# Performance work log

Measured on AMD Instinct MI355X. Metric: run time of the kernel, lower is better.

## Reference

```python
import jax, jax.numpy as jnp
import numpy as np

B, T = 256, 512
LATENT, COND, HID, OUT = 128, 32, 512, 64
IN_DIM = OUT + COND  # LSTM input dim = output_dim + condition_dim


def setup_inputs() -> dict:
    key = jax.random.key(0)
    ks = jax.random.split(key, 14)
    def lin(k, fan_in, shape):
        return jax.random.uniform(k, shape, jnp.float32, -1.0, 1.0) / np.sqrt(fan_in)
    return {
        "latent_vector": jax.random.normal(ks[0], (B, LATENT), jnp.float32),
        "conditions": jax.random.normal(ks[1], (B, COND), jnp.float32),
        "target_sequences": jax.random.normal(ks[2], (B, T, OUT), jnp.float32),
        # latent_to_hidden / latent_to_cell
        "W_lh": lin(ks[3], LATENT, (HID, LATENT)), "b_lh": lin(ks[4], LATENT, (HID,)),
        "W_lc": lin(ks[5], LATENT, (HID, LATENT)), "b_lc": lin(ks[6], LATENT, (HID,)),
        # LSTM weights, torch gate order [i, f, g, o]
        "W_ih": lin(ks[7], HID, (4 * HID, IN_DIM)), "W_hh": lin(ks[8], HID, (4 * HID, HID)),
        "b_ih": lin(ks[9], HID, (4 * HID,)), "b_hh": lin(ks[10], HID, (4 * HID,)),
        # hidden_to_output
        "W_out": lin(ks[11], HID, (OUT, HID)), "b_out": lin(ks[12], HID, (OUT,)),
        "output_lengths": jnp.full((B,), T, dtype=jnp.int32),
    }


def _decode(latent_vector, conditions, target_sequences,
            W_lh, b_lh, W_lc, b_lc, W_ih, W_hh, b_ih, b_hh, W_out, b_out):
    Bb = latent_vector.shape[0]
    Tm = target_sequences.shape[1]  # == output_lengths.max(), static under jit
    D = target_sequences.shape[-1]
    h0 = latent_vector @ W_lh.T + b_lh  # (B, H)
    c0 = latent_vector @ W_lc.T + b_lc  # (B, H)
    init = jnp.ones((Bb, 1, D), target_sequences.dtype)  # initial SOH = 1
    # Teacher forcing (sampling_probability=1.0): step t (t=1..Tm-1) consumes
    # ones at t=1, target[:, t-1] afterwards -> inputs known upfront.
    prev = jnp.concatenate([init, target_sequences[:, 1:Tm - 1, :]], axis=1)  # (B, Tm-1, D)
    cond = jnp.broadcast_to(conditions[:, None, :], (Bb, Tm - 1, conditions.shape[-1]))
    xs = jnp.concatenate([prev, cond], axis=-1)  # (B, Tm-1, D+C)
    # Precompute input contribution to gates for all steps (one big GEMM).
    gx = jnp.einsum('btd,gd->tbg', xs, W_ih) + (b_ih + b_hh)  # (Tm-1, B, 4H)

    def step(carry, g_t):
        h, c = carry
        g = g_t + h @ W_hh.T
        i, f, gg, o = jnp.split(g, 4, axis=-1)
        c = jax.nn.sigmoid(f) * c + jax.nn.sigmoid(i) * jnp.tanh(gg)
        h = jax.nn.sigmoid(o) * jnp.tanh(c)
        return (h, c), h

    _, hs = jax.lax.scan(step, (h0, c0), gx)  # hs: (Tm-1, B, H)
    preds = jnp.einsum('tbh,dh->btd', hs, W_out) + b_out  # (B, Tm-1, D)
    return jnp.concatenate([init, preds], axis=1)  # (B, Tm, D)


def reference(latent_vector, conditions, target_sequences,
              W_lh, b_lh, W_lc, b_lc, W_ih, W_hh, b_ih, b_hh, W_out, b_out,
              output_lengths):
    # output_lengths are all == T; max length is static for jit.
    return _decode(latent_vector, conditions, target_sequences,
                   W_lh, b_lh, W_lc, b_lc, W_ih, W_hh, b_ih, b_hh, W_out, b_out)
```

## Files before the change

### kernel.cpp

```cpp
#include <hip/hip_runtime.h>

#define Bx    256
#define Tx    512
#define LAT   128
#define CND   32
#define HIDN  512
#define OUTD  64
#define KD    608
#define KP    616
#define ROWS  32
#define NCOLS 32

typedef unsigned short u16;
typedef unsigned int   u32;
typedef unsigned long long u64;
typedef short s16x8 __attribute__((ext_vector_type(8)));
typedef unsigned short u16x8 __attribute__((ext_vector_type(8)));
typedef unsigned short u16x4 __attribute__((ext_vector_type(4)));
typedef float f32x4 __attribute__((ext_vector_type(4)));

#define WG_SLICE (NCOLS * KP * 2)
#define WG_OFF   0
#define WG_BYTES (64 * WG_SLICE)
#define H0_OFF   (WG_BYTES)
#define H1_OFF   (H0_OFF + Bx * HIDN * 2)
#define CB_OFF   (H1_OFF + Bx * HIDN * 2)
#define BS_OFF   (CB_OFF + Bx * HIDN * 4)
#define DN_OFF   (BS_OFF + 4 * HIDN * 4)

#define A_BYTES  (ROWS * KP * 2)
#define SMEM_SZ  (2 * A_BYTES + HIDN * 4)
#define WCHUNK   (A_BYTES / 16)
#define RB       1232

__device__ __forceinline__ float sigmoidf_(float x) { return 1.0f / (1.0f + __expf(-x)); }

__device__ __forceinline__ u16 f2bf(float f) {
    union { float f; u32 u; } v; v.f = f;
    u32 r = (v.u + 0x7FFFu + ((v.u >> 16) & 1u)) >> 16;
    return (u16)r;
}
__device__ __forceinline__ float bf2f(u16 s) {
    union { u32 u; float f; } v; v.u = ((u32)s) << 16;
    return v.f;
}
__device__ __forceinline__ void gl_lds16(const void* g, void* l) {
    __builtin_amdgcn_global_load_lds(
        (const __attribute__((address_space(1))) unsigned int*)g,
        (__attribute__((address_space(3))) unsigned int*)l, 16, 0, 0);
}
__device__ __forceinline__ u32 agent_ld(const u32* p) {
    return __hip_atomic_load(p, __ATOMIC_RELAXED, __HIP_MEMORY_SCOPE_AGENT);
}
__device__ __forceinline__ void agent_st(u32* p, u32 v) {
    __hip_atomic_store(p, v, __ATOMIC_RELAXED, __HIP_MEMORY_SCOPE_AGENT);
}
__device__ __forceinline__ u64 agent_ld64(const u64* p) {
    return __hip_atomic_load(p, __ATOMIC_RELAXED, __HIP_MEMORY_SCOPE_AGENT);
}
__device__ __forceinline__ void agent_st64(u64* p, u64 v) {
    __hip_atomic_store(p, v, __ATOMIC_RELAXED, __HIP_MEMORY_SCOPE_AGENT);
}

__global__ __launch_bounds__(256) void prep_w(
    const float* __restrict__ W_ih, const float* __restrict__ W_hh,
    const float* __restrict__ b_ih, const float* __restrict__ b_hh,
    u16* __restrict__ Wg, float* __restrict__ bsum, u32* __restrict__ done_arr)
{
    const int idx = blockIdx.x * 256 + threadIdx.x;
    if (idx < 64 * NCOLS * KD) {
        const int k   = idx % KD;
        const int t   = idx / KD;
        const int col = t % NCOLS;
        const int hs  = t / NCOLS;
        const int g = col >> 3, u = col & 7;
        const int n = g * HIDN + hs * 8 + u;
        const float v = (k < 96) ? W_ih[n * 96 + k] : W_hh[n * HIDN + (k - 96)];
        Wg[(hs * NCOLS + col) * KP + k] = f2bf(v);
    }
    if (idx < 4 * HIDN)  bsum[idx] = b_ih[idx] + b_hh[idx];
    if (idx < 8 * 64 * 4) done_arr[idx] = 0u;
}

__global__ __launch_bounds__(256) void init_kernel(
    const float* __restrict__ latent, const float* __restrict__ W_lh,
    const float* __restrict__ b_lh,   const float* __restrict__ W_lc,
    const float* __restrict__ b_lc,   u16* __restrict__ h0,
    float* __restrict__ c0,           float* __restrict__ out)
{
    const int b = blockIdx.x;
    const float4* lat4 = reinterpret_cast<const float4*>(latent + b * LAT);
#pragma unroll
    for (int jj = 0; jj < 2; ++jj) {
        const int j = threadIdx.x + jj * 256;
        const float4* wh4 = reinterpret_cast<const float4*>(W_lh + j * LAT);
        const float4* wc4 = reinterpret_cast<const float4*>(W_lc + j * LAT);
        float sh = 0.f, sc = 0.f;
#pragma unroll 8
        for (int k = 0; k < LAT / 4; ++k) {
            float4 l = lat4[k], a = wh4[k], c = wc4[k];
            sh += l.x * a.x + l.y * a.y + l.z * a.z + l.w * a.w;
            sc += l.x * c.x + l.y * c.y + l.z * c.z + l.w * c.w;
        }
        h0[b * HIDN + j] = f2bf(sh + b_lh[j]);
        c0[b * HIDN + j] = sc + b_lc[j];
    }
    if (threadIdx.x < OUTD) out[b * (Tx * OUTD) + threadIdx.x] = 1.0f;
}

__global__ __launch_bounds__(256, 2) void persist_kernel(
    const float* __restrict__ target, const float* __restrict__ cond,
    u16* __restrict__ hbuf0, u16* __restrict__ hbuf1,
    const float* __restrict__ cbuf, const u16* __restrict__ Wg,
    const float* __restrict__ bsum, const float* __restrict__ W_out,
    const float* __restrict__ b_out, float* __restrict__ out,
    u32* __restrict__ done)
{
    const int tid  = threadIdx.x;
    const int bs   = blockIdx.x & 7;
    const int hs   = blockIdx.x >> 3;
    const int w    = tid >> 6;
    const int lane = tid & 63;

    __shared__ __align__(16) char smem[SMEM_SZ];
    u16*   As = (u16*)smem;
    u16*   Ws = (u16*)(smem + A_BYTES);
    float* Wo = (float*)(smem + 2 * A_BYTES);

    {
        const u16* wsrc = Wg + hs * (NCOLS * KP);
#pragma unroll
        for (int it = 0; it < 10; ++it) {
            const int base = it * 256 + w * 64;
            if (base + lane < WCHUNK)
                gl_lds16(wsrc + (base + lane) * 8, (void*)(Ws + base * 8));
        }
    }
    if (tid < 128)
        reinterpret_cast<float4*>(Wo)[tid] =
            reinterpret_cast<const float4*>(W_out + hs * HIDN)[tid];

    const int r_  = tid >> 3, q_ = tid & 7;
    const int gb_ = bs * ROWS + r_;
    const int hu_ = hs * 8 + q_;
    float c_reg = cbuf[gb_ * HIDN + hu_];
    const float bsum0 = bsum[0 * HIDN + hu_];
    const float bsum1 = bsum[1 * HIDN + hu_];
    const float bsum2 = bsum[2 * HIDN + hu_];
    const float bsum3 = bsum[3 * HIDN + hu_];
    const float bo    = b_out[hs];

    u16x4 cond_bf;
    {
        const float4 cv = *reinterpret_cast<const float4*>(cond + gb_ * CND + q_ * 4);
        cond_bf[0] = f2bf(cv.x); cond_bf[1] = f2bf(cv.y);
        cond_bf[2] = f2bf(cv.z); cond_bf[3] = f2bf(cv.w);
    }

    const int c2 = tid & 127;
    const int rh = tid >> 7;
    const u64* fpp = (const u64*)(done + ((bs * 64 + (c2 >> 1)) << 2) + (rh << 1));

    const int mrow = ((w & 1) << 4) + (lane & 15);
    const int ncol = ((w >> 1) << 4) + (lane & 15);
    const int kq   = (lane >> 4) << 3;
    const u16* ap  = As + mrow * KP + kq;
    const u16* bp  = Ws + ncol * KP + kq;
    const int row0 = ((w & 1) << 4) + ((lane >> 4) << 2);

    for (int j = 0; j < Tx; ++j) {
        if (j < Tx - 1) {
            u16x8 xv;
            if (j == 0) {
#pragma unroll
                for (int m = 0; m < 8; ++m) xv[m] = 0x3F80;
            } else {
                const float* tg = target + (gb_ * Tx + j) * OUTD + q_ * 8;
                const float4 t0 = *reinterpret_cast<const float4*>(tg);
                const float4 t1 = *reinterpret_cast<const float4*>(tg + 4);
                xv[0]=f2bf(t0.x); xv[1]=f2bf(t0.y); xv[2]=f2bf(t0.z); xv[3]=f2bf(t0.w);
                xv[4]=f2bf(t1.x); xv[5]=f2bf(t1.y); xv[6]=f2bf(t1.z); xv[7]=f2bf(t1.w);
            }
            *reinterpret_cast<u16x8*>(As + r_ * KP + q_ * 8)      = xv;
            *reinterpret_cast<u16x4*>(As + r_ * KP + 64 + q_ * 4) = cond_bf;
        }

        {
            const u32 jj = (u32)j;
            u64 f = agent_ld64(fpp);
            while ((u32)f < jj || (u32)(f >> 32) < jj) f = agent_ld64(fpp);
        }
        {
            const u64* hb = (const u64*)((j & 1) ? hbuf1 : hbuf0);
            const u64* hp = hb + (size_t)(bs * ROWS + rh * 16) * 128 + c2;
            u64 v[16];
#pragma unroll
            for (int m = 0; m < 16; ++m) v[m] = agent_ld64(hp + (size_t)m * 128);
#pragma unroll
            for (int m = 0; m < 16; ++m)
                *reinterpret_cast<u64*>(As + (rh * 16 + m) * KP + 96 + c2 * 4) = v[m];
        }
        __syncthreads();

        if (j == Tx - 1) {
            const u16*   hrow = As + r_ * KP + 96 + q_ * 64;
            const float* wo   = Wo + q_ * 64;
            float p = 0.f;
#pragma unroll
            for (int i = 0; i < 8; ++i) {
                const int ii = (i + q_) & 7;
                u16x8 hv  = *reinterpret_cast<const u16x8*>(hrow + ii * 8);
                float4 w0 = *reinterpret_cast<const float4*>(wo + ii * 8);
                float4 w1 = *reinterpret_cast<const float4*>(wo + ii * 8 + 4);
                p += bf2f(hv[0])*w0.x + bf2f(hv[1])*w0.y + bf2f(hv[2])*w0.z + bf2f(hv[3])*w0.w
                   + bf2f(hv[4])*w1.x + bf2f(hv[5])*w1.y + bf2f(hv[6])*w1.z + bf2f(hv[7])*w1.w;
            }
            p += __shfl_xor(p, 1); p += __shfl_xor(p, 2); p += __shfl_xor(p, 4);
            if (q_ == 0) out[gb_ * (Tx * OUTD) + j * OUTD + hs] = p + bo;
            break;
        }

        f32x4 acc = {0.f, 0.f, 0.f, 0.f};
#pragma unroll
        for (int ck = 0; ck < 19; ++ck) {
            s16x8 a = *reinterpret_cast<const s16x8*>(ap + ck * 32);
            s16x8 b = *reinterpret_cast<const s16x8*>(bp + ck * 32);
            acc = __builtin_amdgcn_mfma_f32_16x16x32_bf16(a, b, acc, 0, 0, 0);
        }
        __syncthreads();
#pragma unroll
        for (int t = 0; t < 4; ++t)
            reinterpret_cast<float*>(smem + (size_t)(row0 + t) * RB)[ncol] = acc[t];
        __syncthreads();

        {
            const float* gr = reinterpret_cast<const float*>(smem + (size_t)r_ * RB);
            const float gi = gr[     q_] + bsum0;
            const float gf = gr[ 8 + q_] + bsum1;
            const float gg = gr[16 + q_] + bsum2;
            const float go = gr[24 + q_] + bsum3;
            const float ig = sigmoidf_(gi), fg = sigmoidf_(gf);
            const float gt = tanhf(gg),     og = sigmoidf_(go);
            c_reg = fg * c_reg + ig * gt;
            const u32 hbit = (u32)f2bf(og * tanhf(c_reg));
            const u32 pair = hbit | ((u32)__shfl_xor((int)hbit, 1) << 16);
            const u64 quad = (u64)pair |
                             ((u64)(u32)__shfl_xor((int)pair, 2) << 32);
            if ((q_ & 3) == 0) {
                u64* hn = (u64*)((j & 1) ? hbuf0 : hbuf1);
                agent_st64(hn + (size_t)gb_ * 128 + hs * 2 + (q_ >> 2), quad);
            }
        }
        asm volatile("s_waitcnt vmcnt(0)" ::: "memory");
        if (lane == 0)
            agent_st(done + ((bs * 64 + hs) << 2) + w, (u32)(j + 1));

        if (j >= 1) {
            const u16*   hrow = As + r_ * KP + 96 + q_ * 64;
            const float* wo   = Wo + q_ * 64;
            float p = 0.f;
#pragma unroll
            for (int i = 0; i < 8; ++i) {
                const int ii = (i + q_) & 7;
                u16x8 hv  = *reinterpret_cast<const u16x8*>(hrow + ii * 8);
                float4 w0 = *reinterpret_cast<const float4*>(wo + ii * 8);
                float4 w1 = *reinterpret_cast<const float4*>(wo + ii * 8 + 4);
                p += bf2f(hv[0])*w0.x + bf2f(hv[1])*w0.y + bf2f(hv[2])*w0.z + bf2f(hv[3])*w0.w
                   + bf2f(hv[4])*w1.x + bf2f(hv[5])*w1.y + bf2f(hv[6])*w1.z + bf2f(hv[7])*w1.w;
            }
            p += __shfl_xor(p, 1); p += __shfl_xor(p, 2); p += __shfl_xor(p, 4);
            if (q_ == 0) out[gb_ * (Tx * OUTD) + j * OUTD + hs] = p + bo;
        }
        __syncthreads();
    }
}

__global__ __launch_bounds__(256, 2) void step_kernel(
    int j,
    const float* __restrict__ target, const float* __restrict__ cond,
    const u16* __restrict__ hprev,    u16* __restrict__ hnext,
    float* __restrict__ cbuf,         const u16* __restrict__ Wg,
    const float* __restrict__ bsum,
    const float* __restrict__ W_out,  const float* __restrict__ b_out,
    float* __restrict__ out)
{
    const int tid  = threadIdx.x;
    const int bs   = blockIdx.x >> 6;
    const int hs   = blockIdx.x & 63;
    const int w    = tid >> 6;
    const int lane = tid & 63;

    if (j >= 1) {
        const int r = tid >> 3, q = tid & 7;
        const int gb = bs * ROWS + r;
        const u16*   hp = hprev + gb * HIDN + q * 64;
        const float* wo = W_out + hs * HIDN + q * 64;
        float p = 0.f;
#pragma unroll
        for (int i = 0; i < 8; ++i) {
            u16x8 hv = *reinterpret_cast<const u16x8*>(hp + i * 8);
            float4 w0 = *reinterpret_cast<const float4*>(wo + i * 8);
            float4 w1 = *reinterpret_cast<const float4*>(wo + i * 8 + 4);
            p += bf2f(hv[0]) * w0.x + bf2f(hv[1]) * w0.y + bf2f(hv[2]) * w0.z + bf2f(hv[3]) * w0.w
               + bf2f(hv[4]) * w1.x + bf2f(hv[5]) * w1.y + bf2f(hv[6]) * w1.z + bf2f(hv[7]) * w1.w;
        }
        p += __shfl_xor(p, 1); p += __shfl_xor(p, 2); p += __shfl_xor(p, 4);
        if (q == 0) out[gb * (Tx * OUTD) + j * OUTD + hs] = p + b_out[hs];
    }
    if (j >= Tx - 1) return;

    __shared__ __align__(16) char smem[2 * ROWS * KP * 2 + 1536];
    u16*   As   = (u16*)smem;
    u16*   Ws   = (u16*)(smem + ROWS * KP * 2);
    float* gbuf = (float*)smem;

    {
        const int r = tid >> 3, t8 = tid & 7;
        const int gb = bs * ROWS + r;
        const float* tg = target + (gb * Tx + j) * OUTD;
#pragma unroll
        for (int m = 0; m < 12; ++m) {
            const int k = t8 * 12 + m;
            float v;
            if (k < OUTD) v = (j == 0) ? 1.0f : tg[k];
            else          v = cond[gb * CND + (k - OUTD)];
            As[r * KP + k] = f2bf(v);
        }
    }
#pragma unroll
    for (int it = 0; it < 8; ++it) {
        const int rr = w + it * 4;
        gl_lds16(hprev + (bs * ROWS + rr) * HIDN + lane * 8, (void*)(As + rr * KP + 96));
    }
    {
        const u16* wsrc = Wg + hs * (NCOLS * KP);
#pragma unroll
        for (int it = 0; it < 10; ++it) {
            const int seg = it * 256 + w * 64;
            gl_lds16(wsrc + seg * 8 + lane * 8, (void*)(Ws + seg * 8));
        }
    }
    __syncthreads();

    const int mrow = ((w & 1) << 4) + (lane & 15);
    const int ncol = ((w >> 1) << 4) + (lane & 15);
    const int kq   = (lane >> 4) << 3;
    const u16* ap = As + mrow * KP + kq;
    const u16* bp = Ws + ncol * KP + kq;
    f32x4 acc = {0.f, 0.f, 0.f, 0.f};
#pragma unroll
    for (int ck = 0; ck < 19; ++ck) {
        s16x8 a = *reinterpret_cast<const s16x8*>(ap + ck * 32);
        s16x8 b = *reinterpret_cast<const s16x8*>(bp + ck * 32);
        acc = __builtin_amdgcn_mfma_f32_16x16x32_bf16(a, b, acc, 0, 0, 0);
    }
    __syncthreads();

    {
        const int row0 = ((w & 1) << 4) + ((lane >> 4) << 2);
#pragma unroll
        for (int t = 0; t < 4; ++t) gbuf[(row0 + t) * 36 + ncol] = acc[t];
    }
    __syncthreads();

    {
        const int r = tid >> 3, u = tid & 7;
        const int gb = bs * ROWS + r, hu = hs * 8 + u;
        const float gi = gbuf[r * 36 +      u] + bsum[0 * HIDN + hu];
        const float gf = gbuf[r * 36 +  8 + u] + bsum[1 * HIDN + hu];
        const float gg = gbuf[r * 36 + 16 + u] + bsum[2 * HIDN + hu];
        const float go = gbuf[r * 36 + 24 + u] + bsum[3 * HIDN + hu];
        const float ig = sigmoidf_(gi), fg = sigmoidf_(gf);
        const float gt = tanhf(gg),     og = sigmoidf_(go);
        const float co = cbuf[gb * HIDN + hu];
        const float cn = fg * co + ig * gt;
        cbuf[gb * HIDN + hu]  = cn;
        hnext[gb * HIDN + hu] = f2bf(og * tanhf(cn));
    }
}

extern "C" void kernel_launch(void* const* d_in, const int* in_sizes, int n_in,
                              void* d_out, int out_size, void* d_ws, size_t ws_size,
                              hipStream_t stream) {
    const float* latent = (const float*)d_in[0];
    const float* cond   = (const float*)d_in[1];
    const float* target = (const float*)d_in[2];
    const float* W_lh   = (const float*)d_in[3];
    const float* b_lh   = (const float*)d_in[4];
    const float* W_lc   = (const float*)d_in[5];
    const float* b_lc   = (const float*)d_in[6];
    const float* W_ih   = (const float*)d_in[7];
    const float* W_hh   = (const float*)d_in[8];
    const float* b_ih   = (const float*)d_in[9];
    const float* b_hh   = (const float*)d_in[10];
    const float* W_out  = (const float*)d_in[11];
    const float* b_out  = (const float*)d_in[12];

    float* out = (float*)d_out;
    char*  ws  = (char*)d_ws;
    u16*   Wg    = (u16*)(ws + WG_OFF);
    u16*   hbuf0 = (u16*)(ws + H0_OFF);
    u16*   hbuf1 = (u16*)(ws + H1_OFF);
    float* cbuf  = (float*)(ws + CB_OFF);
    float* bsum  = (float*)(ws + BS_OFF);
    u32*   done  = (u32*)(ws + DN_OFF);

    hipLaunchKernelGGL(prep_w, dim3(4864), dim3(256), 0, stream,
                       W_ih, W_hh, b_ih, b_hh, Wg, bsum, done);
    hipLaunchKernelGGL(init_kernel, dim3(Bx), dim3(256), 0, stream,
                       latent, W_lh, b_lh, W_lc, b_lc, hbuf0, cbuf, out);

    {
        const float* t_  = target;  const float* c_  = cond;
        u16*         h0_ = hbuf0;   u16*         h1_ = hbuf1;
        const float* cb_ = cbuf;    const u16*   wg_ = Wg;
        const float* bs_ = bsum;    const float* wo_ = W_out;
        const float* bo_ = b_out;   float*       o_  = out;
        u32*         dn_ = done;
        void* args[] = { &t_, &c_, &h0_, &h1_, &cb_, &wg_, &bs_, &wo_, &bo_, &o_, &dn_ };
        hipError_t err = hipLaunchCooperativeKernel(
            reinterpret_cast<const void*>(persist_kernel),
            dim3(512), dim3(256), args, 0, stream);
        if (err != hipSuccess) {
            for (int j = 0; j < Tx; ++j) {
                u16* hp = (j & 1) ? hbuf1 : hbuf0;
                u16* hn = (j & 1) ? hbuf0 : hbuf1;
                hipLaunchKernelGGL(step_kernel, dim3(512), dim3(256), 0, stream,
                                   j, target, cond, hp, hn, cbuf,
                                   Wg, bsum, W_out, b_out, out);
            }
        }
    }
}
```

Before: 2.314 ms.

## Halve persistent grid to 256 blocks, each computing 16 hidden units via dynamic LDS

The persistent cooperative LSTM kernel now runs 256 blocks instead of 512. Each block owns 16 hidden units (64 gate columns) for 32 batch rows, does two MFMA tiles per wave that share one B fragment, and stages gates in a dedicated LDS buffer that needs one fewer barrier. Fewer blocks mean fewer per-step flag polls and less cross-block synchronisation, and the step-0 wait is skipped. In exchange each block holds a weight slice twice as large in dynamic LDS, which forces one block per CU, and the non-cooperative fallback now reads a separately laid-out second weight copy.

```diff
diff --git a/kernel.cpp b/kernel.cpp
--- a/kernel.cpp
+++ b/kernel.cpp
@@ -19,19 +19,20 @@
 typedef unsigned short u16x4 __attribute__((ext_vector_type(4)));
 typedef float f32x4 __attribute__((ext_vector_type(4)));
 
-#define WG_SLICE (NCOLS * KP * 2)
+#define WG_BYTES (2048 * KP * 2)
 #define WG_OFF   0
-#define WG_BYTES (64 * WG_SLICE)
-#define H0_OFF   (WG_BYTES)
+#define WG2_OFF  (WG_BYTES)
+#define H0_OFF   (WG2_OFF + WG_BYTES)
 #define H1_OFF   (H0_OFF + Bx * HIDN * 2)
 #define CB_OFF   (H1_OFF + Bx * HIDN * 2)
 #define BS_OFF   (CB_OFF + Bx * HIDN * 4)
 #define DN_OFF   (BS_OFF + 4 * HIDN * 4)
 
-#define A_BYTES  (ROWS * KP * 2)
-#define SMEM_SZ  (2 * A_BYTES + HIDN * 4)
-#define WCHUNK   (A_BYTES / 16)
-#define RB       1232
+#define PA_BYTES 39424
+#define PW_BYTES 78848
+#define PO_BYTES 4096
+#define PG_BYTES 8704
+#define PSMEM    (PA_BYTES + PW_BYTES + PO_BYTES + PG_BYTES)
 
 __device__ __forceinline__ float sigmoidf_(float x) { return 1.0f / (1.0f + __expf(-x)); }
 
@@ -65,21 +66,25 @@
 __global__ __launch_bounds__(256) void prep_w(
     const float* __restrict__ W_ih, const float* __restrict__ W_hh,
     const float* __restrict__ b_ih, const float* __restrict__ b_hh,
-    u16* __restrict__ Wg, float* __restrict__ bsum, u32* __restrict__ done_arr)
+    u16* __restrict__ Wg, u16* __restrict__ Wg2,
+    float* __restrict__ bsum, u32* __restrict__ done_arr)
 {
     const int idx = blockIdx.x * 256 + threadIdx.x;
-    if (idx < 64 * NCOLS * KD) {
+    if (idx < 2048 * KD) {
         const int k   = idx % KD;
         const int t   = idx / KD;
-        const int col = t % NCOLS;
-        const int hs  = t / NCOLS;
-        const int g = col >> 3, u = col & 7;
-        const int n = g * HIDN + hs * 8 + u;
+        const int col = t & 63;
+        const int hs  = t >> 6;
+        const int g = col >> 4, u = col & 15;
+        const int n = g * HIDN + hs * 16 + u;
         const float v = (k < 96) ? W_ih[n * 96 + k] : W_hh[n * HIDN + (k - 96)];
-        Wg[(hs * NCOLS + col) * KP + k] = f2bf(v);
-    }
-    if (idx < 4 * HIDN)  bsum[idx] = b_ih[idx] + b_hh[idx];
-    if (idx < 8 * 64 * 4) done_arr[idx] = 0u;
+        const u16 b = f2bf(v);
+        Wg[(hs * 64 + col) * KP + k] = b;
+        const int nn = n & 511;
+        Wg2[(((nn >> 3) * 32) + g * 8 + (nn & 7)) * KP + k] = b;
+    }
+    if (idx < 4 * HIDN)   bsum[idx] = b_ih[idx] + b_hh[idx];
+    if (idx < 8 * 32 * 4) done_arr[idx] = 0u;
 }
 
 __global__ __launch_bounds__(256) void init_kernel(
@@ -108,7 +113,7 @@
     if (threadIdx.x < OUTD) out[b * (Tx * OUTD) + threadIdx.x] = 1.0f;
 }
 
-__global__ __launch_bounds__(256, 2) void persist_kernel(
+__global__ __launch_bounds__(256, 1) void persist_kernel(
     const float* __restrict__ target, const float* __restrict__ cond,
     u16* __restrict__ hbuf0, u16* __restrict__ hbuf1,
     const float* __restrict__ cbuf, const u16* __restrict__ Wg,
@@ -122,33 +127,38 @@
     const int w    = tid >> 6;
     const int lane = tid & 63;
 
-    __shared__ __align__(16) char smem[SMEM_SZ];
-    u16*   As = (u16*)smem;
-    u16*   Ws = (u16*)(smem + A_BYTES);
-    float* Wo = (float*)(smem + 2 * A_BYTES);
-
-    {
-        const u16* wsrc = Wg + hs * (NCOLS * KP);
-#pragma unroll
-        for (int it = 0; it < 10; ++it) {
-            const int base = it * 256 + w * 64;
-            if (base + lane < WCHUNK)
-                gl_lds16(wsrc + (base + lane) * 8, (void*)(Ws + base * 8));
-        }
-    }
-    if (tid < 128)
-        reinterpret_cast<float4*>(Wo)[tid] =
-            reinterpret_cast<const float4*>(W_out + hs * HIDN)[tid];
-
-    const int r_  = tid >> 3, q_ = tid & 7;
+    extern __shared__ __align__(16) char smem[];
+    u16*   As   = (u16*)smem;
+    u16*   Ws   = (u16*)(smem + PA_BYTES);
+    float* Wo   = (float*)(smem + PA_BYTES + PW_BYTES);
+    float* gbuf = (float*)(smem + PA_BYTES + PW_BYTES + PO_BYTES);
+
+    {
+        const u16* wsrc = Wg + hs * (64 * KP);
+#pragma unroll
+        for (int it = 0; it < 20; ++it) {
+            const int c = it * 256 + tid;
+            if (c < PW_BYTES / 16) gl_lds16(wsrc + c * 8, (void*)(Ws + c * 8));
+        }
+    }
+    reinterpret_cast<float4*>(Wo)[tid] =
+        reinterpret_cast<const float4*>(W_out + (hs * 2) * HIDN)[tid];
+
+    const int u_   = tid & 15;
+    const int rr   = tid >> 4;
+    const int row0c = 2 * rr, row1c = 2 * rr + 1;
+    const int gbr0 = bs * ROWS + row0c;
+    const int hu_  = hs * 16 + u_;
+    float c0r = cbuf[gbr0 * HIDN + hu_];
+    float c1r = cbuf[(gbr0 + 1) * HIDN + hu_];
+    const float bsm0 = bsum[0 * HIDN + hu_];
+    const float bsm1 = bsum[1 * HIDN + hu_];
+    const float bsm2 = bsum[2 * HIDN + hu_];
+    const float bsm3 = bsum[3 * HIDN + hu_];
+
+    const int r_ = tid >> 3, q_ = tid & 7;
     const int gb_ = bs * ROWS + r_;
-    const int hu_ = hs * 8 + q_;
-    float c_reg = cbuf[gb_ * HIDN + hu_];
-    const float bsum0 = bsum[0 * HIDN + hu_];
-    const float bsum1 = bsum[1 * HIDN + hu_];
-    const float bsum2 = bsum[2 * HIDN + hu_];
-    const float bsum3 = bsum[3 * HIDN + hu_];
-    const float bo    = b_out[hs];
+    const float bo0 = b_out[hs * 2], bo1 = b_out[hs * 2 + 1];
 
     u16x4 cond_bf;
     {
@@ -159,14 +169,15 @@
 
     const int c2 = tid & 127;
     const int rh = tid >> 7;
-    const u64* fpp = (const u64*)(done + ((bs * 64 + (c2 >> 1)) << 2) + (rh << 1));
-
-    const int mrow = ((w & 1) << 4) + (lane & 15);
-    const int ncol = ((w >> 1) << 4) + (lane & 15);
+    const u64* fpp = (const u64*)(done + ((bs * 32 + (c2 >> 2)) << 2) + (rh << 1));
+
+    const int ml   = lane & 15;
+    const int ncol = w * 16 + ml;
     const int kq   = (lane >> 4) << 3;
-    const u16* ap  = As + mrow * KP + kq;
+    const u16* ap0 = As + ml * KP + kq;
+    const u16* ap1 = As + (16 + ml) * KP + kq;
     const u16* bp  = Ws + ncol * KP + kq;
-    const int row0 = ((w & 1) << 4) + ((lane >> 4) << 2);
+    const int  sr0 = (lane >> 4) << 2;
 
     for (int j = 0; j < Tx; ++j) {
         if (j < Tx - 1) {
@@ -185,7 +196,7 @@
             *reinterpret_cast<u16x4*>(As + r_ * KP + 64 + q_ * 4) = cond_bf;
         }
 
-        {
+        if (j > 0) {
             const u32 jj = (u32)j;
             u64 f = agent_ld64(fpp);
             while ((u32)f < jj || (u32)(f >> 32) < jj) f = agent_ld64(fpp);
@@ -203,73 +214,95 @@
         __syncthreads();
 
         if (j == Tx - 1) {
-            const u16*   hrow = As + r_ * KP + 96 + q_ * 64;
-            const float* wo   = Wo + q_ * 64;
-            float p = 0.f;
+            const u16* hrow = As + r_ * KP + 96 + q_ * 64;
+            float p0 = 0.f, p1 = 0.f;
 #pragma unroll
             for (int i = 0; i < 8; ++i) {
                 const int ii = (i + q_) & 7;
-                u16x8 hv  = *reinterpret_cast<const u16x8*>(hrow + ii * 8);
-                float4 w0 = *reinterpret_cast<const float4*>(wo + ii * 8);
-                float4 w1 = *reinterpret_cast<const float4*>(wo + ii * 8 + 4);
-                p += bf2f(hv[0])*w0.x + bf2f(hv[1])*w0.y + bf2f(hv[2])*w0.z + bf2f(hv[3])*w0.w
-                   + bf2f(hv[4])*w1.x + bf2f(hv[5])*w1.y + bf2f(hv[6])*w1.z + bf2f(hv[7])*w1.w;
-            }
-            p += __shfl_xor(p, 1); p += __shfl_xor(p, 2); p += __shfl_xor(p, 4);
-            if (q_ == 0) out[gb_ * (Tx * OUTD) + j * OUTD + hs] = p + bo;
+                u16x8 hv = *reinterpret_cast<const u16x8*>(hrow + ii * 8);
+                const float* wo0 = Wo + q_ * 64 + ii * 8;
+                const float* wo1 = Wo + 512 + q_ * 64 + ii * 8;
+#pragma unroll
+                for (int m = 0; m < 8; ++m) {
+                    const float hf = bf2f(hv[m]);
+                    p0 += hf * wo0[m]; p1 += hf * wo1[m];
+                }
+            }
+            p0 += __shfl_xor(p0, 1); p0 += __shfl_xor(p0, 2); p0 += __shfl_xor(p0, 4);
+            p1 += __shfl_xor(p1, 1); p1 += __shfl_xor(p1, 2); p1 += __shfl_xor(p1, 4);
+            if (q_ == 0) {
+                float* op = out + gb_ * (Tx * OUTD) + j * OUTD + hs * 2;
+                op[0] = p0 + bo0; op[1] = p1 + bo1;
+            }
             break;
         }
 
-        f32x4 acc = {0.f, 0.f, 0.f, 0.f};
+        f32x4 acc0 = {0.f, 0.f, 0.f, 0.f};
+        f32x4 acc1 = {0.f, 0.f, 0.f, 0.f};
 #pragma unroll
         for (int ck = 0; ck < 19; ++ck) {
-            s16x8 a = *reinterpret_cast<const s16x8*>(ap + ck * 32);
-            s16x8 b = *reinterpret_cast<const s16x8*>(bp + ck * 32);
-            acc = __builtin_amdgcn_mfma_f32_16x16x32_bf16(a, b, acc, 0, 0, 0);
+            s16x8 a0 = *reinterpret_cast<const s16x8*>(ap0 + ck * 32);
+            s16x8 a1 = *reinterpret_cast<const s16x8*>(ap1 + ck * 32);
+            s16x8 b  = *reinterpret_cast<const s16x8*>(bp  + ck * 32);
+            acc0 = __builtin_amdgcn_mfma_f32_16x16x32_bf16(a0, b, acc0, 0, 0, 0);
+            acc1 = __builtin_amdgcn_mfma_f32_16x16x32_bf16(a1, b, acc1, 0, 0, 0);
+        }
+#pragma unroll
+        for (int t = 0; t < 4; ++t) {
+            gbuf[(sr0 + t) * 68 + ncol]        = acc0[t];
+            gbuf[(sr0 + t + 16) * 68 + ncol]   = acc1[t];
         }
         __syncthreads();
-#pragma unroll
-        for (int t = 0; t < 4; ++t)
-            reinterpret_cast<float*>(smem + (size_t)(row0 + t) * RB)[ncol] = acc[t];
-        __syncthreads();
 
         {
-            const float* gr = reinterpret_cast<const float*>(smem + (size_t)r_ * RB);
-            const float gi = gr[     q_] + bsum0;
-            const float gf = gr[ 8 + q_] + bsum1;
-            const float gg = gr[16 + q_] + bsum2;
-            const float go = gr[24 + q_] + bsum3;
-            const float ig = sigmoidf_(gi), fg = sigmoidf_(gf);
-            const float gt = tanhf(gg),     og = sigmoidf_(go);
-            c_reg = fg * c_reg + ig * gt;
-            const u32 hbit = (u32)f2bf(og * tanhf(c_reg));
-            const u32 pair = hbit | ((u32)__shfl_xor((int)hbit, 1) << 16);
-            const u64 quad = (u64)pair |
-                             ((u64)(u32)__shfl_xor((int)pair, 2) << 32);
-            if ((q_ & 3) == 0) {
+            const float gi0 = gbuf[row0c * 68 +      u_] + bsm0;
+            const float gf0 = gbuf[row0c * 68 + 16 + u_] + bsm1;
+            const float gg0 = gbuf[row0c * 68 + 32 + u_] + bsm2;
+            const float go0 = gbuf[row0c * 68 + 48 + u_] + bsm3;
+            const float gi1 = gbuf[row1c * 68 +      u_] + bsm0;
+            const float gf1 = gbuf[row1c * 68 + 16 + u_] + bsm1;
+            const float gg1 = gbuf[row1c * 68 + 32 + u_] + bsm2;
+            const float go1 = gbuf[row1c * 68 + 48 + u_] + bsm3;
+            c0r = sigmoidf_(gf0) * c0r + sigmoidf_(gi0) * tanhf(gg0);
+            c1r = sigmoidf_(gf1) * c1r + sigmoidf_(gi1) * tanhf(gg1);
+            const u32 h0b = (u32)f2bf(sigmoidf_(go0) * tanhf(c0r));
+            const u32 h1b = (u32)f2bf(sigmoidf_(go1) * tanhf(c1r));
+            const u32 p0 = h0b | ((u32)__shfl_xor((int)h0b, 1) << 16);
+            const u32 p1 = h1b | ((u32)__shfl_xor((int)h1b, 1) << 16);
+            const u64 q0 = (u64)p0 | ((u64)(u32)__shfl_xor((int)p0, 2) << 32);
+            const u64 q1 = (u64)p1 | ((u64)(u32)__shfl_xor((int)p1, 2) << 32);
+            if ((u_ & 3) == 0) {
                 u64* hn = (u64*)((j & 1) ? hbuf0 : hbuf1);
-                agent_st64(hn + (size_t)gb_ * 128 + hs * 2 + (q_ >> 2), quad);
+                u64* a = hn + (size_t)gbr0 * 128 + hs * 4 + (u_ >> 2);
+                agent_st64(a, q0);
+                agent_st64(a + 128, q1);
             }
         }
         asm volatile("s_waitcnt vmcnt(0)" ::: "memory");
         if (lane == 0)
-            agent_st(done + ((bs * 64 + hs) << 2) + w, (u32)(j + 1));
+            agent_st(done + ((bs * 32 + hs) << 2) + w, (u32)(j + 1));
 
         if (j >= 1) {
-            const u16*   hrow = As + r_ * KP + 96 + q_ * 64;
-            const float* wo   = Wo + q_ * 64;
-            float p = 0.f;
+            const u16* hrow = As + r_ * KP + 96 + q_ * 64;
+            float p0 = 0.f, p1 = 0.f;
 #pragma unroll
             for (int i = 0; i < 8; ++i) {
                 const int ii = (i + q_) & 7;
-                u16x8 hv  = *reinterpret_cast<const u16x8*>(hrow + ii * 8);
-                float4 w0 = *reinterpret_cast<const float4*>(wo + ii * 8);
-                float4 w1 = *reinterpret_cast<const float4*>(wo + ii * 8 + 4);
-                p += bf2f(hv[0])*w0.x + bf2f(hv[1])*w0.y + bf2f(hv[2])*w0.z + bf2f(hv[3])*w0.w
-                   + bf2f(hv[4])*w1.x + bf2f(hv[5])*w1.y + bf2f(hv[6])*w1.z + bf2f(hv[7])*w1.w;
-            }
-            p += __shfl_xor(p, 1); p += __shfl_xor(p, 2); p += __shfl_xor(p, 4);
-            if (q_ == 0) out[gb_ * (Tx * OUTD) + j * OUTD + hs] = p + bo;
+                u16x8 hv = *reinterpret_cast<const u16x8*>(hrow + ii * 8);
+                const float* wo0 = Wo + q_ * 64 + ii * 8;
+                const float* wo1 = Wo + 512 + q_ * 64 + ii * 8;
+#pragma unroll
+                for (int m = 0; m < 8; ++m) {
+                    const float hf = bf2f(hv[m]);
+                    p0 += hf * wo0[m]; p1 += hf * wo1[m];
+                }
+            }
+            p0 += __shfl_xor(p0, 1); p0 += __shfl_xor(p0, 2); p0 += __shfl_xor(p0, 4);
+            p1 += __shfl_xor(p1, 1); p1 += __shfl_xor(p1, 2); p1 += __shfl_xor(p1, 4);
+            if (q_ == 0) {
+                float* op = out + gb_ * (Tx * OUTD) + j * OUTD + hs * 2;
+                op[0] = p0 + bo0; op[1] = p1 + bo1;
+            }
         }
         __syncthreads();
     }
@@ -399,6 +432,7 @@
     float* out = (float*)d_out;
     char*  ws  = (char*)d_ws;
     u16*   Wg    = (u16*)(ws + WG_OFF);
+    u16*   Wg2   = (u16*)(ws + WG2_OFF);
     u16*   hbuf0 = (u16*)(ws + H0_OFF);
     u16*   hbuf1 = (u16*)(ws + H1_OFF);
     float* cbuf  = (float*)(ws + CB_OFF);
@@ -406,11 +440,13 @@
     u32*   done  = (u32*)(ws + DN_OFF);
 
     hipLaunchKernelGGL(prep_w, dim3(4864), dim3(256), 0, stream,
-                       W_ih, W_hh, b_ih, b_hh, Wg, bsum, done);
+                       W_ih, W_hh, b_ih, b_hh, Wg, Wg2, bsum, done);
     hipLaunchKernelGGL(init_kernel, dim3(Bx), dim3(256), 0, stream,
                        latent, W_lh, b_lh, W_lc, b_lc, hbuf0, cbuf, out);
 
     {
+        (void)hipFuncSetAttribute(reinterpret_cast<const void*>(persist_kernel),
+                                  hipFuncAttributeMaxDynamicSharedMemorySize, PSMEM);
         const float* t_  = target;  const float* c_  = cond;
         u16*         h0_ = hbuf0;   u16*         h1_ = hbuf1;
         const float* cb_ = cbuf;    const u16*   wg_ = Wg;
@@ -420,15 +456,15 @@
         void* args[] = { &t_, &c_, &h0_, &h1_, &cb_, &wg_, &bs_, &wo_, &bo_, &o_, &dn_ };
         hipError_t err = hipLaunchCooperativeKernel(
             reinterpret_cast<const void*>(persist_kernel),
-            dim3(512), dim3(256), args, 0, stream);
+            dim3(256), dim3(256), args, PSMEM, stream);
         if (err != hipSuccess) {
             for (int j = 0; j < Tx; ++j) {
                 u16* hp = (j & 1) ? hbuf1 : hbuf0;
                 u16* hn = (j & 1) ? hbuf0 : hbuf1;
                 hipLaunchKernelGGL(step_kernel, dim3(512), dim3(256), 0, stream,
                                    j, target, cond, hp, hn, cbuf,
-                                   Wg, bsum, W_out, b_out, out);
-            }
-        }
-    }
-}
+                                   Wg2, bsum, W_out, b_out, out);
+            }
+        }
+    }
+}
```

Result: faster. 2.255 ms (-2.5%).
